# Kernel optimization log

Hardware: AMD Instinct MI355X
Metric: run time of the kernel (lower is better)

Reference implementation:

```python
import jax, jax.numpy as jnp
import numpy as np

B, S, D = 2, 2048, 2048
HQ, HKV, HD = 16, 4, 128
EPS = 1e-8


def _rope_tables(seq_len, dim, base=10000.0):
    inv_freq = 1.0 / (base ** (jnp.arange(0, dim, 2, dtype=jnp.float32) / dim))
    freqs = jnp.outer(jnp.arange(seq_len, dtype=jnp.float32), inv_freq)  # S x dim/2
    emb = jnp.concatenate([freqs, freqs], axis=-1)  # S x dim
    return jnp.cos(emb), jnp.sin(emb)


def setup_inputs() -> dict:
    key = jax.random.key(0)
    ks = jax.random.split(key, 6)
    cos_theta, sin_theta = _rope_tables(S, HD)
    return {
        "x": jax.random.normal(ks[0], (B, S, D), dtype=jnp.float32),
        "Wq": jax.random.normal(ks[1], (D, HQ * HD), dtype=jnp.float32) * 0.02,
        "Wk": jax.random.normal(ks[2], (D, HKV * HD), dtype=jnp.float32) * 0.02,
        "Wv": jax.random.normal(ks[3], (D, HKV * HD), dtype=jnp.float32) * 0.02,
        "Wo": jax.random.normal(ks[4], (HQ * HD, D), dtype=jnp.float32) * 0.02,
        "q_norm_w": jnp.zeros((HD,), dtype=jnp.float32),
        "k_norm_w": jnp.zeros((HD,), dtype=jnp.float32),
        "cos_theta": cos_theta,
        "sin_theta": sin_theta,
        "padding_mask": jnp.zeros((B, S), dtype=bool),
        "window_size": 1024,
    }


def _rmsnorm(x, w):
    return x * jax.lax.rsqrt(jnp.mean(x * x, axis=-1, keepdims=True) + EPS) * (1.0 + w)


def _rotate_half(x):
    x1, x2 = jnp.split(x, 2, axis=-1)
    return jnp.concatenate([-x2, x1], axis=-1)


def _rope(x, cos_t, sin_t):
    # x: B x H x S x d; cos/sin: S x d
    return x * cos_t[None, None] + _rotate_half(x) * sin_t[None, None]


def reference(x, Wq, Wk, Wv, Wo, q_norm_w, k_norm_w, cos_theta, sin_theta, padding_mask, window_size):
    b, s, _ = x.shape
    scale = HD ** -0.5
    q = (x @ Wq).reshape(b, s, HQ, HD).transpose(0, 2, 1, 3)   # b,HQ,s,d
    k = (x @ Wk).reshape(b, s, HKV, HD).transpose(0, 2, 1, 3)  # b,HKV,s,d
    v = (x @ Wv).reshape(b, s, HKV, HD).transpose(0, 2, 1, 3)
    q = _rope(_rmsnorm(q, q_norm_w), cos_theta[:s], sin_theta[:s])
    k = _rope(_rmsnorm(k, k_norm_w), cos_theta[:s], sin_theta[:s])

    # causal & sliding window & padding mask
    qi = jnp.arange(s)[:, None]
    ki = jnp.arange(s)[None, :]
    mask = (qi >= ki) & ((qi - ki) <= window_size)          # s x s
    pad = padding_mask[:, :, None] | padding_mask[:, None, :]  # b x s x s
    mask = mask[None] & ~pad                                 # b x s x s

    g = HQ // HKV
    qg = q.reshape(b, HKV, g, s, HD)
    scores = jnp.einsum('bngqd,bnkd->bngqk', qg, k) * scale  # b,HKV,g,s,s
    scores = jnp.where(mask[:, None, None], scores, -jnp.inf)
    attn = jax.nn.softmax(scores, axis=-1)
    out = jnp.einsum('bngqk,bnkd->bngqd', attn, v)
    out = out.reshape(b, HQ, s, HD).transpose(0, 2, 1, 3).reshape(b, s, HQ * HD)
    return out @ Wo
```

## Files before the change

kernel.cpp:

```cpp
#include <hip/hip_runtime.h>

typedef __attribute__((ext_vector_type(4))) float f32x4;
typedef __attribute__((ext_vector_type(8))) __bf16 bf16x8;
typedef __attribute__((ext_vector_type(4))) __bf16 bf16x4;

__device__ __forceinline__ void gload_lds16(const __bf16* g, __bf16* l) {
  __builtin_amdgcn_global_load_lds(
      (const __attribute__((address_space(1))) unsigned int*)(g),
      (__attribute__((address_space(3))) unsigned int*)(l), 16, 0, 0);
}

__global__ __launch_bounds__(256) void prep(
    const float* __restrict__ Wq, const float* __restrict__ Wk,
    const float* __restrict__ Wv, const float* __restrict__ Wo,
    const float4* __restrict__ x, const unsigned long long* __restrict__ pad,
    __bf16* __restrict__ Wqkvt, __bf16* __restrict__ Wot,
    bf16x4* __restrict__ xb, unsigned char* __restrict__ pad64) {
  const int bx = blockIdx.x, by = blockIdx.y;
  const int tx = threadIdx.x, ty = threadIdx.y;
  const int tid = ty * 32 + tx;
  if (bx >= 160) {
    int i = ((bx - 160) * 64 + by) * 256 + tid;
    float4 v = x[i];
    bf16x4 o = {(__bf16)v.x, (__bf16)v.y, (__bf16)v.z, (__bf16)v.w};
    xb[i] = o;
    return;
  }
  if (bx == 0 && by == 0 && tid < 64) {
    unsigned long long acc = 0;
#pragma unroll
    for (int i = 0; i < 8; ++i) acc |= pad[tid * 8 + i];
    pad64[tid] = (acc != 0) ? 1 : 0;
  }
  __shared__ float t[32][33];
  const float* src; __bf16* dst; int ss, c0;
  if (bx < 64)      { src = Wq; dst = Wqkvt;                       ss = 2048; c0 = bx * 32; }
  else if (bx < 80) { src = Wk; dst = Wqkvt + (size_t)2048 * 2048; ss = 512;  c0 = (bx - 64) * 32; }
  else if (bx < 96) { src = Wv; dst = Wqkvt + (size_t)2560 * 2048; ss = 512;  c0 = (bx - 80) * 32; }
  else              { src = Wo; dst = Wot;                         ss = 2048; c0 = (bx - 96) * 32; }
  const int r0 = by * 32;
#pragma unroll
  for (int i = ty; i < 32; i += 8)
    t[i][tx] = src[(size_t)(r0 + i) * ss + c0 + tx];
  __syncthreads();
#pragma unroll
  for (int i = ty; i < 32; i += 8)
    dst[(size_t)(c0 + i) * 2048 + r0 + tx] = (__bf16)t[tx][i];
}

__global__ __launch_bounds__(256) void gemm_qkv(
    const __bf16* __restrict__ A, const __bf16* __restrict__ Bt,
    __bf16* __restrict__ Qb, __bf16* __restrict__ Kb, __bf16* __restrict__ Vt) {
  __shared__ __align__(16) __bf16 smem[128 * 136];
  __bf16* As = smem;
  __bf16* Bs = smem + 128 * 32;
  __bf16* stage = smem;
  const int K = 2048;
  const int tid = threadIdx.x;
  const int lane = tid & 63;
  const int c15 = lane & 15, quad = lane >> 4;
  const int wm = ((tid >> 6) & 1) * 64;
  const int wn = (tid >> 7) * 64;
  const int jb = blockIdx.x;
  const int m0 = blockIdx.y * 128, n0 = jb * 128;
  const int wbase = tid & 192;

  f32x4 acc[4][4] = {};

  const int row0 = tid >> 2, cc0 = (tid & 3) * 8;
  const int row1 = (tid + 256) >> 2;
  const __bf16* a0 = A + (size_t)(m0 + row0) * K + cc0;
  const __bf16* a1 = A + (size_t)(m0 + row1) * K + cc0;
  const __bf16* b0 = Bt + (size_t)(n0 + row0) * K + cc0;
  const __bf16* b1 = Bt + (size_t)(n0 + row1) * K + cc0;
  __bf16* lA0 = As + (size_t)wbase * 8;
  __bf16* lA1 = As + (size_t)(256 + wbase) * 8;
  __bf16* lB0 = Bs + (size_t)wbase * 8;
  __bf16* lB1 = Bs + (size_t)(256 + wbase) * 8;

  for (int k0 = 0; k0 < K; k0 += 32) {
    gload_lds16(a0 + k0, lA0);
    gload_lds16(a1 + k0, lA1);
    gload_lds16(b0 + k0, lB0);
    gload_lds16(b1 + k0, lB1);
    __syncthreads();
    bf16x8 af[4], bfr[4];
#pragma unroll
    for (int i = 0; i < 4; ++i) {
      af[i]  = *(const bf16x8*)(As + (wm + i * 16 + c15) * 32 + quad * 8);
      bfr[i] = *(const bf16x8*)(Bs + (wn + i * 16 + c15) * 32 + quad * 8);
    }
#pragma unroll
    for (int i = 0; i < 4; ++i)
#pragma unroll
      for (int j = 0; j < 4; ++j)
        acc[i][j] = __builtin_amdgcn_mfma_f32_16x16x32_bf16(af[i], bfr[j], acc[i][j], 0, 0, 0);
    __syncthreads();
  }

  const int b = m0 >> 11;
  const int s0 = m0 & 2047;
  const int orow = tid >> 4, ocol = (tid & 15) * 8;

  if (jb >= 20) {
#pragma unroll
    for (int j = 0; j < 4; ++j) {
      int d = wn + j * 16 + c15;
#pragma unroll
      for (int i = 0; i < 4; ++i) {
        int sl = wm + i * 16 + quad * 4;
        bf16x4 o = {(__bf16)acc[i][j][0], (__bf16)acc[i][j][1],
                    (__bf16)acc[i][j][2], (__bf16)acc[i][j][3]};
        *(bf16x4*)(stage + (size_t)d * 136 + sl) = o;
      }
    }
    __syncthreads();
    __bf16* VtH = Vt + (((size_t)b * 4 + (jb - 20)) * 128) * 2048;
#pragma unroll
    for (int p = 0; p < 8; ++p) {
      int d = p * 16 + orow;
      *(bf16x8*)(VtH + (size_t)d * 2048 + s0 + ocol) =
          *(const bf16x8*)(stage + (size_t)d * 136 + ocol);
    }
    return;
  }

#pragma unroll
  for (int i = 0; i < 4; ++i)
#pragma unroll
    for (int j = 0; j < 4; ++j)
#pragma unroll
      for (int r = 0; r < 4; ++r)
        stage[(size_t)(wm + i * 16 + quad * 4 + r) * 136 + wn + j * 16 + c15] =
            (__bf16)acc[i][j][r];
  __syncthreads();
  __bf16* dstH = (jb < 16) ? Qb + (((size_t)b * 16 + jb) * 2048) * 128
                           : Kb + (((size_t)b * 4 + (jb - 16)) * 2048) * 128;
#pragma unroll
  for (int p = 0; p < 8; ++p) {
    int sl = p * 16 + orow;
    *(bf16x8*)(dstH + (size_t)(s0 + sl) * 128 + ocol) =
        *(const bf16x8*)(stage + (size_t)sl * 136 + ocol);
  }
}

__global__ __launch_bounds__(256) void norm_rope(
    __bf16* __restrict__ Qb, __bf16* __restrict__ Kb,
    const float* __restrict__ qw, const float* __restrict__ kw,
    const float* __restrict__ cosT, const float* __restrict__ sinT) {
  const int tid = threadIdx.x, w = tid >> 6, lane = tid & 63;
  const int v = blockIdx.x * 4 + w;
  const bool isQ = v < 65536;
  __bf16* base = isQ ? Qb + (size_t)v * 128 : Kb + (size_t)(v - 65536) * 128;
  const int s = v & 2047;
  float x1 = (float)base[lane], x2 = (float)base[lane + 64];
  float ss = x1 * x1 + x2 * x2;
#pragma unroll
  for (int d = 32; d; d >>= 1) ss += __shfl_xor(ss, d);
  float rn = rsqrtf(ss * (1.0f / 128.0f) + 1e-8f);
  const float* wt = isQ ? qw : kw;
  float n1 = x1 * rn * (1.0f + wt[lane]);
  float n2 = x2 * rn * (1.0f + wt[lane + 64]);
  float c1 = cosT[s * 128 + lane], c2 = cosT[s * 128 + 64 + lane];
  float s1 = sinT[s * 128 + lane], s2 = sinT[s * 128 + 64 + lane];
  const float QSC = 0.08838834764831845f * 1.4426950408889634f;
  float post = isQ ? QSC : 1.0f;
  base[lane]      = (__bf16)((n1 * c1 - n2 * s1) * post);
  base[lane + 64] = (__bf16)((n2 * c2 + n1 * s2) * post);
}

__global__ __launch_bounds__(256) void gemm_bt(const __bf16* __restrict__ A,
                                               const __bf16* __restrict__ Bt,
                                               float* __restrict__ C,
                                               int M, int N, int K) {
  __shared__ __align__(16) __bf16 As[128 * 32];
  __shared__ __align__(16) __bf16 Bs[128 * 32];
  const int tid = threadIdx.x;
  const int lane = tid & 63;
  const int c15 = lane & 15, quad = lane >> 4;
  const int wm = ((tid >> 6) & 1) * 64;
  const int wn = (tid >> 7) * 64;
  const int m0 = blockIdx.y * 128, n0 = blockIdx.x * 128;
  const int wbase = tid & 192;

  f32x4 acc[4][4] = {};

  const int row0 = tid >> 2, cc0 = (tid & 3) * 8;
  const int row1 = (tid + 256) >> 2;
  const __bf16* a0 = A + (size_t)(m0 + row0) * K + cc0;
  const __bf16* a1 = A + (size_t)(m0 + row1) * K + cc0;
  const __bf16* b0 = Bt + (size_t)(n0 + row0) * K + cc0;
  const __bf16* b1 = Bt + (size_t)(n0 + row1) * K + cc0;
  __bf16* lA0 = As + (size_t)wbase * 8;
  __bf16* lA1 = As + (size_t)(256 + wbase) * 8;
  __bf16* lB0 = Bs + (size_t)wbase * 8;
  __bf16* lB1 = Bs + (size_t)(256 + wbase) * 8;

  for (int k0 = 0; k0 < K; k0 += 32) {
    gload_lds16(a0 + k0, lA0);
    gload_lds16(a1 + k0, lA1);
    gload_lds16(b0 + k0, lB0);
    gload_lds16(b1 + k0, lB1);
    __syncthreads();
    bf16x8 af[4], bfr[4];
#pragma unroll
    for (int i = 0; i < 4; ++i) {
      af[i]  = *(const bf16x8*)(As + (wm + i * 16 + c15) * 32 + quad * 8);
      bfr[i] = *(const bf16x8*)(Bs + (wn + i * 16 + c15) * 32 + quad * 8);
    }
#pragma unroll
    for (int i = 0; i < 4; ++i)
#pragma unroll
      for (int j = 0; j < 4; ++j)
        acc[i][j] = __builtin_amdgcn_mfma_f32_16x16x32_bf16(af[i], bfr[j], acc[i][j], 0, 0, 0);
    __syncthreads();
  }

#pragma unroll
  for (int i = 0; i < 4; ++i) {
    int r0 = m0 + wm + i * 16 + quad * 4;
#pragma unroll
    for (int j = 0; j < 4; ++j) {
      int cc = n0 + wn + j * 16 + c15;
#pragma unroll
      for (int r = 0; r < 4; ++r)
        C[(size_t)(r0 + r) * N + cc] = acc[i][j][r];
    }
  }
}

__global__ __launch_bounds__(256) void attn(
    const __bf16* __restrict__ Qb, const __bf16* __restrict__ Kb,
    const __bf16* __restrict__ Vt, const unsigned char* __restrict__ pad,
    const unsigned char* __restrict__ pad64, const int* __restrict__ winp,
    __bf16* __restrict__ O) {
  const int S = 2048;
  __shared__ __align__(16) __bf16 Ks[64 * 128];
  __shared__ __align__(16) __bf16 Vs[128 * 64];
  __shared__ __align__(16) __bf16 Ps[4 * 32 * 72];
  const int tid = threadIdx.x, w = tid >> 6, lane = tid & 63;
  const int c15 = lane & 15, quad = lane >> 4;
  const int b = blockIdx.z;
  const int bx = (b == 0) ? blockIdx.x : (gridDim.x - 1 - blockIdx.x);
  const int q0 = ((int)gridDim.x - 1 - bx) * 32;
  const int kv = blockIdx.y;
  const int h = kv * 4 + w;
  const int W = *winp;
  const unsigned char* padb = pad + (size_t)b * S;
  const unsigned char* pad64b = pad64 + b * 32;
  const __bf16* Qh = Qb + (((size_t)b * 16 + h) * S) * 128;
  const __bf16* Kh = Kb + (((size_t)b * 4 + kv) * S) * 128;
  const __bf16* Vh = Vt + (((size_t)b * 4 + kv) * 128) * (size_t)S;
  __bf16* Pw = Ps + w * 32 * 72;

  bf16x8 qf0[4], qf1[4];
#pragma unroll
  for (int c = 0; c < 4; ++c) {
    qf0[c] = *(const bf16x8*)(Qh + (size_t)(q0 + c15) * 128 + c * 32 + quad * 8);
    qf1[c] = *(const bf16x8*)(Qh + (size_t)(q0 + 16 + c15) * 128 + c * 32 + quad * 8);
  }

  f32x4 acc0[8] = {}, acc1[8] = {};
  float lsum0[4] = {0.f, 0.f, 0.f, 0.f};
  float lsum1[4] = {0.f, 0.f, 0.f, 0.f};

  const int krow_i = lane >> 4, kch = lane & 15;
  const int vrow_i = lane >> 3, vch = lane & 7;

  int kb0 = q0 - W; if (kb0 < 0) kb0 = 0; kb0 &= ~63;

  for (int kb = kb0; kb <= q0 + 31; kb += 64) {
    __syncthreads();
#pragma unroll
    for (int i = 0; i < 4; ++i) {
      int row = w * 16 + i * 4 + krow_i;
      gload_lds16(Kh + (size_t)(kb + row) * 128 + ((kch ^ (row & 15)) * 8),
                  Ks + (w * 16 + i * 4) * 128);
    }
#pragma unroll
    for (int i = 0; i < 4; ++i) {
      int row = w * 32 + i * 8 + vrow_i;
      gload_lds16(Vh + (size_t)row * S + kb + ((vch ^ (row & 7)) * 8),
                  Vs + (w * 32 + i * 8) * 64);
    }
    __syncthreads();

    f32x4 sf0[4], sf1[4];
#pragma unroll
    for (int nb = 0; nb < 4; ++nb) {
      f32x4 ca = {}, cb = {};
#pragma unroll
      for (int c = 0; c < 4; ++c) {
        bf16x8 kf = *(const bf16x8*)(Ks + (nb * 16 + c15) * 128 + (((c * 4 + quad) ^ c15) * 8));
        ca = __builtin_amdgcn_mfma_f32_16x16x32_bf16(qf0[c], kf, ca, 0, 0, 0);
        cb = __builtin_amdgcn_mfma_f32_16x16x32_bf16(qf1[c], kf, cb, 0, 0, 0);
      }
      sf0[nb] = ca; sf1[nb] = cb;
    }

    const bool fast = (kb + 63 <= q0) && (q0 + 31 - kb <= W) && (pad64b[kb >> 6] == 0);
    if (fast) {
#pragma unroll
      for (int r = 0; r < 4; ++r) {
        float a0 = exp2f(sf0[0][r]), a1 = exp2f(sf0[1][r]);
        float a2 = exp2f(sf0[2][r]), a3 = exp2f(sf0[3][r]);
        lsum0[r] += (a0 + a1) + (a2 + a3);
        int pr = (quad * 4 + r) * 72 + c15;
        Pw[pr] = (__bf16)a0; Pw[pr + 16] = (__bf16)a1;
        Pw[pr + 32] = (__bf16)a2; Pw[pr + 48] = (__bf16)a3;
        float b0 = exp2f(sf1[0][r]), b1 = exp2f(sf1[1][r]);
        float b2 = exp2f(sf1[2][r]), b3 = exp2f(sf1[3][r]);
        lsum1[r] += (b0 + b1) + (b2 + b3);
        int qr = pr + 16 * 72;
        Pw[qr] = (__bf16)b0; Pw[qr + 16] = (__bf16)b1;
        Pw[qr + 32] = (__bf16)b2; Pw[qr + 48] = (__bf16)b3;
      }
    } else {
#pragma unroll
      for (int r = 0; r < 4; ++r) {
        const int qi0 = q0 + quad * 4 + r;
        const int qi1 = qi0 + 16;
        float p0[4], p1[4];
#pragma unroll
        for (int nb = 0; nb < 4; ++nb) {
          int ki = kb + nb * 16 + c15;
          bool okp = (padb[ki] == 0);
          bool ok0 = (ki <= qi0) && ((qi0 - ki) <= W) && okp;
          bool ok1 = (ki <= qi1) && ((qi1 - ki) <= W) && okp;
          float e0 = exp2f(sf0[nb][r]);
          float e1 = exp2f(sf1[nb][r]);
          p0[nb] = ok0 ? e0 : 0.0f;
          p1[nb] = ok1 ? e1 : 0.0f;
        }
        lsum0[r] += (p0[0] + p0[1]) + (p0[2] + p0[3]);
        lsum1[r] += (p1[0] + p1[1]) + (p1[2] + p1[3]);
        int pr = (quad * 4 + r) * 72 + c15;
        Pw[pr] = (__bf16)p0[0]; Pw[pr + 16] = (__bf16)p0[1];
        Pw[pr + 32] = (__bf16)p0[2]; Pw[pr + 48] = (__bf16)p0[3];
        int qr = pr + 16 * 72;
        Pw[qr] = (__bf16)p1[0]; Pw[qr + 16] = (__bf16)p1[1];
        Pw[qr + 32] = (__bf16)p1[2]; Pw[qr + 48] = (__bf16)p1[3];
      }
    }

    bf16x8 pf00 = *(const bf16x8*)(Pw + c15 * 72 + quad * 8);
    bf16x8 pf01 = *(const bf16x8*)(Pw + c15 * 72 + 32 + quad * 8);
    bf16x8 pf10 = *(const bf16x8*)(Pw + (16 + c15) * 72 + quad * 8);
    bf16x8 pf11 = *(const bf16x8*)(Pw + (16 + c15) * 72 + 32 + quad * 8);
#pragma unroll
    for (int nb = 0; nb < 8; ++nb) {
      int row = nb * 16 + c15;
      bf16x8 vf0 = *(const bf16x8*)(Vs + row * 64 + ((quad ^ (c15 & 7)) * 8));
      bf16x8 vf1 = *(const bf16x8*)(Vs + row * 64 + (((4 + quad) ^ (c15 & 7)) * 8));
      acc0[nb] = __builtin_amdgcn_mfma_f32_16x16x32_bf16(pf00, vf0, acc0[nb], 0, 0, 0);
      acc0[nb] = __builtin_amdgcn_mfma_f32_16x16x32_bf16(pf01, vf1, acc0[nb], 0, 0, 0);
      acc1[nb] = __builtin_amdgcn_mfma_f32_16x16x32_bf16(pf10, vf0, acc1[nb], 0, 0, 0);
      acc1[nb] = __builtin_amdgcn_mfma_f32_16x16x32_bf16(pf11, vf1, acc1[nb], 0, 0, 0);
    }
  }

#pragma unroll
  for (int r = 0; r < 4; ++r) {
    lsum0[r] += __shfl_xor(lsum0[r], 1);
    lsum0[r] += __shfl_xor(lsum0[r], 2);
    lsum0[r] += __shfl_xor(lsum0[r], 4);
    lsum0[r] += __shfl_xor(lsum0[r], 8);
    lsum1[r] += __shfl_xor(lsum1[r], 1);
    lsum1[r] += __shfl_xor(lsum1[r], 2);
    lsum1[r] += __shfl_xor(lsum1[r], 4);
    lsum1[r] += __shfl_xor(lsum1[r], 8);
  }
  float inv0[4], inv1[4];
#pragma unroll
  for (int r = 0; r < 4; ++r) { inv0[r] = 1.0f / lsum0[r]; inv1[r] = 1.0f / lsum1[r]; }
#pragma unroll
  for (int nb = 0; nb < 8; ++nb)
#pragma unroll
    for (int r = 0; r < 4; ++r) {
      size_t idx = ((size_t)b * S + q0 + quad * 4 + r) * 2048 + h * 128 + nb * 16 + c15;
      O[idx] = (__bf16)(acc0[nb][r] * inv0[r]);
      O[idx + (size_t)16 * 2048] = (__bf16)(acc1[nb][r] * inv1[r]);
    }
}

extern "C" void kernel_launch(void* const* d_in, const int* in_sizes, int n_in,
                              void* d_out, int out_size, void* d_ws, size_t ws_size,
                              hipStream_t stream) {
  const float* x    = (const float*)d_in[0];
  const float* Wq   = (const float*)d_in[1];
  const float* Wk   = (const float*)d_in[2];
  const float* Wv   = (const float*)d_in[3];
  const float* Wo   = (const float*)d_in[4];
  const float* qw   = (const float*)d_in[5];
  const float* kw   = (const float*)d_in[6];
  const float* cosT = (const float*)d_in[7];
  const float* sinT = (const float*)d_in[8];
  const unsigned char* pad = (const unsigned char*)d_in[9];
  const int* win    = (const int*)d_in[10];

  char* ws = (char*)d_ws;
  __bf16* xb    = (__bf16*)(ws + 0);
  __bf16* Wqkvt = (__bf16*)(ws + 16777216);
  __bf16* Wot   = (__bf16*)(ws + 29360128);
  __bf16* Qb    = (__bf16*)(ws + 37748736);
  __bf16* Kb    = (__bf16*)(ws + 54525952);
  __bf16* Vt    = (__bf16*)(ws + 58720256);
  __bf16* Ob    = (__bf16*)(ws + 62914560);
  unsigned char* pad64 = (unsigned char*)(ws + 79691776);

  prep<<<dim3(288, 64, 1), dim3(32, 8, 1), 0, stream>>>(
      Wq, Wk, Wv, Wo, (const float4*)x, (const unsigned long long*)pad,
      Wqkvt, Wot, (bf16x4*)xb, pad64);

  gemm_qkv<<<dim3(24, 32, 1), 256, 0, stream>>>(xb, Wqkvt, Qb, Kb, Vt);

  norm_rope<<<20480, 256, 0, stream>>>(Qb, Kb, qw, kw, cosT, sinT);

  attn<<<dim3(64, 4, 2), 256, 0, stream>>>(Qb, Kb, Vt, pad, pad64, win, Ob);

  gemm_bt<<<dim3(16, 32, 1), 256, 0, stream>>>(Ob, Wot, (float*)d_out, 4096, 2048, 2048);
}
```

Baseline: 322.5 us.

## Rewrite QKV GEMM with 256x256 tiles, double-buffered LDS and swizzled layout

```diff
diff --git a/kernel.cpp b/kernel.cpp
--- a/kernel.cpp
+++ b/kernel.cpp
@@ -48,99 +48,127 @@
     dst[(size_t)(c0 + i) * 2048 + r0 + tx] = (__bf16)t[tx][i];
 }
 
-__global__ __launch_bounds__(256) void gemm_qkv(
+__device__ __forceinline__ void stage_t(const __bf16* aS, const __bf16* bS,
+                                        __bf16* Ab, __bf16* Bb, int wb8, size_t kt) {
+#pragma unroll
+  for (int l = 0; l < 4; ++l)
+    gload_lds16(aS + (size_t)l * 131072 + kt, Ab + l * 4096 + wb8);
+#pragma unroll
+  for (int l = 0; l < 4; ++l)
+    gload_lds16(bS + (size_t)l * 131072 + kt, Bb + l * 4096 + wb8);
+}
+
+__global__ __launch_bounds__(512, 2) void gemm_qkv256(
     const __bf16* __restrict__ A, const __bf16* __restrict__ Bt,
     __bf16* __restrict__ Qb, __bf16* __restrict__ Kb, __bf16* __restrict__ Vt) {
-  __shared__ __align__(16) __bf16 smem[128 * 136];
-  __bf16* As = smem;
-  __bf16* Bs = smem + 128 * 32;
-  __bf16* stage = smem;
+  extern __shared__ __bf16 smem[];
   const int K = 2048;
   const int tid = threadIdx.x;
-  const int lane = tid & 63;
+  const int lane = tid & 63, w = tid >> 6;
   const int c15 = lane & 15, quad = lane >> 4;
-  const int wm = ((tid >> 6) & 1) * 64;
-  const int wn = (tid >> 7) * 64;
-  const int jb = blockIdx.x;
-  const int m0 = blockIdx.y * 128, n0 = jb * 128;
-  const int wbase = tid & 192;
-
-  f32x4 acc[4][4] = {};
-
-  const int row0 = tid >> 2, cc0 = (tid & 3) * 8;
-  const int row1 = (tid + 256) >> 2;
-  const __bf16* a0 = A + (size_t)(m0 + row0) * K + cc0;
-  const __bf16* a1 = A + (size_t)(m0 + row1) * K + cc0;
-  const __bf16* b0 = Bt + (size_t)(n0 + row0) * K + cc0;
-  const __bf16* b1 = Bt + (size_t)(n0 + row1) * K + cc0;
-  __bf16* lA0 = As + (size_t)wbase * 8;
-  __bf16* lA1 = As + (size_t)(256 + wbase) * 8;
-  __bf16* lB0 = Bs + (size_t)wbase * 8;
-  __bf16* lB1 = Bs + (size_t)(256 + wbase) * 8;
-
-  for (int k0 = 0; k0 < K; k0 += 32) {
-    gload_lds16(a0 + k0, lA0);
-    gload_lds16(a1 + k0, lA1);
-    gload_lds16(b0 + k0, lB0);
-    gload_lds16(b1 + k0, lB1);
-    __syncthreads();
-    bf16x8 af[4], bfr[4];
-#pragma unroll
-    for (int i = 0; i < 4; ++i) {
-      af[i]  = *(const bf16x8*)(As + (wm + i * 16 + c15) * 32 + quad * 8);
-      bfr[i] = *(const bf16x8*)(Bs + (wn + i * 16 + c15) * 32 + quad * 8);
-    }
-#pragma unroll
-    for (int i = 0; i < 4; ++i)
-#pragma unroll
-      for (int j = 0; j < 4; ++j)
-        acc[i][j] = __builtin_amdgcn_mfma_f32_16x16x32_bf16(af[i], bfr[j], acc[i][j], 0, 0, 0);
-    __syncthreads();
+  const int wm = w >> 2, wn = w & 3;
+  const int id = blockIdx.x;
+  const int swz = (id & 7) * 24 + (id >> 3);
+  const int m0 = (swz / 12) * 256, n0 = (swz % 12) * 256;
+
+  const int srow = tid >> 3;
+  const int scol = ((tid & 7) ^ (srow & 7)) * 8;
+  const __bf16* aSrc = A + (size_t)(m0 + srow) * K + scol;
+  const __bf16* bSrc = Bt + (size_t)(n0 + srow) * K + scol;
+  const int wb8 = (tid & 448) * 8;
+  __bf16* A0 = smem;
+  __bf16* B0 = smem + 16384;
+  __bf16* A1 = smem + 32768;
+  __bf16* B1 = smem + 49152;
+
+  f32x4 acc[8][4] = {};
+
+  stage_t(aSrc, bSrc, A0, B0, wb8, 0);
+  stage_t(aSrc, bSrc, A1, B1, wb8, 64);
+
+  for (int t = 0; t < 32; ++t) {
+    __bf16* Ab = smem + (t & 1) * 32768;
+    __bf16* Bb = Ab + 16384;
+    if (t < 31) asm volatile("s_waitcnt vmcnt(8)" ::: "memory");
+    else        asm volatile("s_waitcnt vmcnt(0)" ::: "memory");
+    __builtin_amdgcn_s_barrier();
+    __builtin_amdgcn_sched_barrier(0);
+
+    bf16x8 bF[4][2];
+#pragma unroll
+    for (int j = 0; j < 4; ++j) {
+      int RB = wn * 64 + j * 16 + c15;
+#pragma unroll
+      for (int h = 0; h < 2; ++h)
+        bF[j][h] = *(const bf16x8*)(Bb + RB * 64 + (((h * 4 + quad) ^ (RB & 7)) * 8));
+    }
+    __builtin_amdgcn_s_setprio(1);
+#pragma unroll
+    for (int i = 0; i < 8; ++i) {
+      int RA = wm * 128 + i * 16 + c15;
+      bf16x8 a0 = *(const bf16x8*)(Ab + RA * 64 + ((quad ^ (RA & 7)) * 8));
+      bf16x8 a1 = *(const bf16x8*)(Ab + RA * 64 + (((4 + quad) ^ (RA & 7)) * 8));
+#pragma unroll
+      for (int j = 0; j < 4; ++j) {
+        acc[i][j] = __builtin_amdgcn_mfma_f32_16x16x32_bf16(a0, bF[j][0], acc[i][j], 0, 0, 0);
+        acc[i][j] = __builtin_amdgcn_mfma_f32_16x16x32_bf16(a1, bF[j][1], acc[i][j], 0, 0, 0);
+      }
+    }
+    __builtin_amdgcn_s_setprio(0);
+    __builtin_amdgcn_sched_barrier(0);
+    asm volatile("s_waitcnt lgkmcnt(0)" ::: "memory");
+    __builtin_amdgcn_s_barrier();
+    __builtin_amdgcn_sched_barrier(0);
+    if (t < 30) stage_t(aSrc, bSrc, Ab, Bb, wb8, (size_t)(t + 2) * 64);
   }
 
   const int b = m0 >> 11;
   const int s0 = m0 & 2047;
-  const int orow = tid >> 4, ocol = (tid & 15) * 8;
-
-  if (jb >= 20) {
-#pragma unroll
-    for (int j = 0; j < 4; ++j) {
-      int d = wn + j * 16 + c15;
-#pragma unroll
-      for (int i = 0; i < 4; ++i) {
-        int sl = wm + i * 16 + quad * 4;
+  const int colbase = n0 + wn * 64;
+  __bf16* st = smem + w * 8192;
+
+  if (colbase >= 2560) {
+#pragma unroll
+    for (int i = 0; i < 8; ++i)
+#pragma unroll
+      for (int j = 0; j < 4; ++j) {
+        int dl = j * 16 + c15;
+        int gr = (i * 2 + (quad >> 1)) ^ (dl & 7);
         bf16x4 o = {(__bf16)acc[i][j][0], (__bf16)acc[i][j][1],
                     (__bf16)acc[i][j][2], (__bf16)acc[i][j][3]};
-        *(bf16x4*)(stage + (size_t)d * 136 + sl) = o;
+        *(bf16x4*)(st + dl * 128 + gr * 8 + (quad & 1) * 4) = o;
       }
-    }
-    __syncthreads();
-    __bf16* VtH = Vt + (((size_t)b * 4 + (jb - 20)) * 128) * 2048;
-#pragma unroll
-    for (int p = 0; p < 8; ++p) {
-      int d = p * 16 + orow;
-      *(bf16x8*)(VtH + (size_t)d * 2048 + s0 + ocol) =
-          *(const bf16x8*)(stage + (size_t)d * 136 + ocol);
-    }
-    return;
-  }
-
-#pragma unroll
-  for (int i = 0; i < 4; ++i)
-#pragma unroll
-    for (int j = 0; j < 4; ++j)
-#pragma unroll
-      for (int r = 0; r < 4; ++r)
-        stage[(size_t)(wm + i * 16 + quad * 4 + r) * 136 + wn + j * 16 + c15] =
-            (__bf16)acc[i][j][r];
-  __syncthreads();
-  __bf16* dstH = (jb < 16) ? Qb + (((size_t)b * 16 + jb) * 2048) * 128
-                           : Kb + (((size_t)b * 4 + (jb - 16)) * 2048) * 128;
-#pragma unroll
-  for (int p = 0; p < 8; ++p) {
-    int sl = p * 16 + orow;
-    *(bf16x8*)(dstH + (size_t)(s0 + sl) * 128 + ocol) =
-        *(const bf16x8*)(stage + (size_t)sl * 136 + ocol);
+    __bf16* VtH = Vt + (((size_t)b * 4 + ((colbase - 2560) >> 7)) * 128) * 2048 +
+                  (size_t)(colbase & 127) * 2048 + s0 + wm * 128;
+#pragma unroll
+    for (int pass = 0; pass < 16; ++pass) {
+      int d = pass * 4 + quad;
+      int gp = (c15 & 8) | ((c15 ^ d) & 7);
+      *(bf16x8*)(VtH + (size_t)d * 2048 + c15 * 8) =
+          *(const bf16x8*)(st + d * 128 + gp * 8);
+    }
+  } else {
+#pragma unroll
+    for (int i = 0; i < 8; ++i)
+#pragma unroll
+      for (int j = 0; j < 4; ++j)
+#pragma unroll
+        for (int r = 0; r < 4; ++r) {
+          int s = i * 16 + quad * 4 + r;
+          int dl = j * 16 + c15;
+          st[s * 64 + (((dl >> 3) ^ (s & 7)) * 8) + (dl & 7)] = (__bf16)acc[i][j][r];
+        }
+    __bf16* dstH = (colbase < 2048)
+        ? Qb + (((size_t)b * 16 + (colbase >> 7)) * 2048) * 128 + (colbase & 127)
+        : Kb + (((size_t)b * 4 + ((colbase - 2048) >> 7)) * 2048) * 128 + (colbase & 127);
+    dstH += (size_t)(s0 + wm * 128) * 128;
+    const int g = lane & 7, sl = lane >> 3;
+#pragma unroll
+    for (int it = 0; it < 16; ++it) {
+      int s = it * 8 + sl;
+      *(bf16x8*)(dstH + (size_t)s * 128 + g * 8) =
+          *(const bf16x8*)(st + s * 64 + ((g ^ (s & 7)) * 8));
+    }
   }
 }
 
@@ -408,11 +436,15 @@
   __bf16* Ob    = (__bf16*)(ws + 62914560);
   unsigned char* pad64 = (unsigned char*)(ws + 79691776);
 
+  static int qkv_attr = (int)hipFuncSetAttribute(
+      (const void*)gemm_qkv256, hipFuncAttributeMaxDynamicSharedMemorySize, 131072);
+  (void)qkv_attr;
+
   prep<<<dim3(288, 64, 1), dim3(32, 8, 1), 0, stream>>>(
       Wq, Wk, Wv, Wo, (const float4*)x, (const unsigned long long*)pad,
       Wqkvt, Wot, (bf16x4*)xb, pad64);
 
-  gemm_qkv<<<dim3(24, 32, 1), 256, 0, stream>>>(xb, Wqkvt, Qb, Kb, Vt);
+  gemm_qkv256<<<dim3(192, 1, 1), 512, 131072, stream>>>(xb, Wqkvt, Qb, Kb, Vt);
 
   norm_rope<<<20480, 256, 0, stream>>>(Qb, Kb, qw, kw, cosT, sinT);
 
```

Result: no change. 322.5 us (+0.0%).
